# Optimization experiments

Hardware: AMD Instinct MI355X
Metric: run time of the kernel (lower is better)

The kernel has to match this reference:

```python
import jax, jax.numpy as jnp
import numpy as np


def _relative_position_index(ws: int) -> np.ndarray:
    # Matches torch meshgrid (ij) construction in _init_relative_positions.
    coords = np.stack(np.meshgrid(np.arange(ws), np.arange(ws), indexing='ij'), axis=0).reshape(2, -1)  # [2, ws*ws]
    rel = coords[:, :, None] - coords[:, None, :]          # [2, N, N]
    rel = rel.transpose(1, 2, 0).copy()                    # [N, N, 2]
    rel[:, :, 0] += ws - 1
    rel[:, :, 1] += ws - 1
    rel[:, :, 0] *= 2 * ws - 1
    return rel.sum(-1)                                     # [N, N] int


def setup_inputs() -> dict:
    key = jax.random.key(0)
    ks = jax.random.split(key, 6)
    B, N, C, H, WS = 4096, 49, 512, 16, 7
    x = jax.random.normal(ks[0], (B, N, C), dtype=jnp.float32)
    w_qkv = jax.random.normal(ks[1], (C, 3 * C), dtype=jnp.float32) * (C ** -0.5)
    b_qkv = jax.random.normal(ks[2], (3 * C,), dtype=jnp.float32) * 0.02
    w_proj = jax.random.normal(ks[3], (C, C), dtype=jnp.float32) * (C ** -0.5)
    b_proj = jax.random.normal(ks[4], (C,), dtype=jnp.float32) * 0.02
    bias_table = jax.random.normal(ks[5], ((2 * WS - 1) ** 2, H), dtype=jnp.float32) * 0.02
    return {"x": x, "w_qkv": w_qkv, "b_qkv": b_qkv, "w_proj": w_proj,
            "b_proj": b_proj, "bias_table": bias_table,
            "num_heads": H, "window_size": WS}


def reference(x, w_qkv, b_qkv, w_proj, b_proj, bias_table, num_heads, window_size):
    B, N, C = x.shape
    hd = C // num_heads
    qkv = (x @ w_qkv + b_qkv).reshape(B, N, 3, num_heads, hd)
    q, k, v = (qkv[:, :, i].transpose(0, 2, 1, 3) for i in range(3))  # each [B, H, N, hd]
    # NOTE: scale uses full channel dim C (as in source), not head_dim.
    attn = jnp.einsum('bhnd,bhmd->bhnm', q, k) * (C ** -0.5)          # [B, H, N, N]
    idx = _relative_position_index(window_size)                        # [N, N] static
    rel_bias = bias_table[idx].transpose(2, 0, 1)                      # [H, N, N]
    attn = jax.nn.softmax(attn + rel_bias[None], axis=-1)
    out = jnp.einsum('bhnm,bhmd->bhnd', attn, v)                       # [B, H, N, hd]
    out = out.transpose(0, 2, 1, 3).reshape(B, N, C)
    return out @ w_proj + b_proj
```

## Files before the change

kernel.cpp:

```cpp
#include <hip/hip_runtime.h>
#include <hip/hip_bf16.h>

typedef __attribute__((ext_vector_type(8))) short bf16x8;
typedef __attribute__((ext_vector_type(4))) float f32x4;

#define DEVI __device__ __forceinline__

DEVI short f2bf(float f) {
  union { float f; unsigned u; } v; v.f = f;
  unsigned r = v.u + 0x7FFFu + ((v.u >> 16) & 1u);
  return (short)(r >> 16);
}

DEVI void gl16(const void* g, void* l) {
  __builtin_amdgcn_global_load_lds((const __attribute__((address_space(1))) unsigned*)g,
                                   (__attribute__((address_space(3))) unsigned*)l,
                                   16, 0, 0);
}

DEVI float exp2a(float x) { float r; asm("v_exp_f32 %0, %1" : "=v"(r) : "v"(x)); return r; }

DEVI unsigned pk2(float lo, float hi) {
  union { __hip_bfloat162 h; unsigned u; } v;
  float2 f; f.x = lo; f.y = hi;
  v.h = __float22bfloat162_rn(f);
  return v.u;
}

union U8 { unsigned u[4]; bf16x8 v; };
DEVI bf16x8 mk8(unsigned a, unsigned b, unsigned c, unsigned d) {
  U8 x; x.u[0]=a; x.u[1]=b; x.u[2]=c; x.u[3]=d; return x.v;
}


__global__ __launch_bounds__(256) void conv_x_k(const float* __restrict__ x,
                                                short* __restrict__ xb) {
  long i = (long)blockIdx.x * 256 + threadIdx.x;
  const float4* xf = (const float4*)x;
  float4 a = xf[i * 2], c = xf[i * 2 + 1];
  bf16x8 r;
  r[0] = f2bf(a.x); r[1] = f2bf(a.y); r[2] = f2bf(a.z); r[3] = f2bf(a.w);
  r[4] = f2bf(c.x); r[5] = f2bf(c.y); r[6] = f2bf(c.z); r[7] = f2bf(c.w);
  *(bf16x8*)(xb + i * 8) = r;
}

__global__ __launch_bounds__(256) void conv_wT_k(const float* __restrict__ w,
                                                 short* __restrict__ wT, int Ncols) {
  int i = blockIdx.x * 256 + threadIdx.x;
  if (i >= Ncols * 512) return;
  int n = i >> 9, k = i & 511;
  wT[i] = f2bf(w[k * Ncols + n]);
}

__global__ __launch_bounds__(256) void fill_biasT(const float* __restrict__ btab,
                                                  float* __restrict__ biasT) {
  int i = blockIdx.x * 256 + threadIdx.x;
  int h = i >> 12, m = (i >> 6) & 63, n = i & 63;
  float v;
  if (m >= 49) {
    v = -1e30f;
  } else {
    int nn = n > 48 ? 48 : n;
    int ni = nn / 7, nj = nn - ni * 7;
    int mi = m / 7,  mj = m - mi * 7;
    int idx = (ni - mi + 6) * 13 + (nj - mj + 6);
    v = btab[idx * 16 + h] * 1.4426950408889634f;
  }
  biasT[i] = v;
}


template <int EPI>
__global__ __launch_bounds__(256, 2)
void gemm128(const short* __restrict__ A, const short* __restrict__ Bt,
             const float* __restrict__ bias, void* __restrict__ outp, int ctiles) {
  __shared__ short As[4096];
  __shared__ short Bs[4096];

  const int nwg = gridDim.x;
  const int w = blockIdx.x;
  const int chunk = nwg >> 3;
  const int tid = (w & 7) * chunk + (w >> 3);
  const int rt = tid / ctiles, ct = tid % ctiles;
  const long m0 = (long)rt * 128;
  const int n0 = ct * 128;

  const int t = threadIdx.x;
  const int lane = t & 63;
  const int wv = t >> 6;
  const int wm = wv >> 1, wn = wv & 1;
  const int l15 = lane & 15, g = lane >> 4;

  const int rA0 = t >> 2, cA = t & 3;
  const short* Ag0 = A + (m0 + rA0) * 512 + cA * 8;
  const short* Ag1 = A + (m0 + rA0 + 64) * 512 + cA * 8;
  const short* Bg0 = Bt + (long)(n0 + rA0) * 512 + cA * 8;
  const short* Bg1 = Bt + (long)(n0 + rA0 + 64) * 512 + cA * 8;
  short* Al0 = As + t * 8;
  short* Al1 = As + (t + 256) * 8;
  short* Bl0 = Bs + t * 8;
  short* Bl1 = Bs + (t + 256) * 8;

  const short* aRd = As + (wm * 64 + l15) * 32 + g * 8;
  const short* bRd = Bs + (wn * 64 + l15) * 32 + g * 8;

  f32x4 acc[4][4] = {};

  for (int kk = 0; kk < 512; kk += 32) {
    __syncthreads();
    gl16(Ag0 + kk, Al0);
    gl16(Ag1 + kk, Al1);
    gl16(Bg0 + kk, Bl0);
    gl16(Bg1 + kk, Bl1);
    __syncthreads();
    bf16x8 a[4], b[4];
#pragma unroll
    for (int i = 0; i < 4; ++i) a[i] = *(const bf16x8*)(aRd + i * 512);
#pragma unroll
    for (int j = 0; j < 4; ++j) b[j] = *(const bf16x8*)(bRd + j * 512);
#pragma unroll
    for (int i = 0; i < 4; ++i)
#pragma unroll
      for (int j = 0; j < 4; ++j)
        acc[i][j] = __builtin_amdgcn_mfma_f32_16x16x32_bf16(a[i], b[j], acc[i][j], 0, 0, 0);
  }

  if (EPI == 0) {
    short* qkv = (short*)outp;
#pragma unroll
    for (int i = 0; i < 4; ++i)
#pragma unroll
      for (int r = 0; r < 4; ++r) {
        int row = (int)m0 + wm * 64 + i * 16 + g * 4 + r;
        int b = row / 49, n = row - b * 49;
#pragma unroll
        for (int j = 0; j < 4; ++j) {
          int col = n0 + wn * 64 + j * 16 + l15;
          float val = acc[i][j][r] + bias[col];
          int ii = col >> 9, h = (col >> 5) & 15, d = col & 31;
          qkv[(long)((b * 16 + h) * 3 + ii) * 1568 + n * 32 + d] = f2bf(val);
        }
      }
  } else {
    float* out = (float*)outp;
#pragma unroll
    for (int i = 0; i < 4; ++i)
#pragma unroll
      for (int r = 0; r < 4; ++r) {
        long row = m0 + wm * 64 + i * 16 + g * 4 + r;
#pragma unroll
        for (int j = 0; j < 4; ++j) {
          int col = n0 + wn * 64 + j * 16 + l15;
          out[row * 512 + col] = acc[i][j][r] + bias[col];
        }
      }
  }
}


__global__ __launch_bounds__(256, 3)
void attn49(const short* __restrict__ qkvb, const float* __restrict__ biasT,
            short* __restrict__ ao) {
  const int t = threadIdx.x, lane = t & 63, wv = t >> 6;
  const int l15 = lane & 15, g = lane >> 4, g4 = g * 4;
  const int b = blockIdx.x >> 2;
  const int h = (blockIdx.x & 3) * 4 + wv;

  const short* qb = qkvb + (long)(b * 16 + h) * 3 * 1568;
  const short* kb = qb + 1568;
  const short* vb = kb + 1568;

  bf16x8 qf[4], kf[4];
#pragma unroll
  for (int i = 0; i < 4; ++i) {
    int row = i * 16 + l15; row = row > 48 ? 48 : row;
    kf[i] = *(const bf16x8*)(kb + row * 32 + g * 8);
    qf[i] = *(const bf16x8*)(qb + row * 32 + g * 8);
  }

  bf16x8 vf[2][2];
#pragma unroll
  for (int kt = 0; kt < 2; ++kt)
#pragma unroll
    for (int hi = 0; hi < 2; ++hi)
#pragma unroll
      for (int r = 0; r < 4; ++r) {
        int m = kt * 32 + hi * 16 + g4 + r;
        m = m > 48 ? 48 : m;
#pragma unroll
        for (int dt = 0; dt < 2; ++dt)
          vf[kt][dt][hi * 4 + r] = vb[m * 32 + dt * 16 + l15];
      }

  f32x4 s[4][4] = {};
#pragma unroll
  for (int i = 0; i < 4; ++i)
#pragma unroll
    for (int j = 0; j < 4; ++j)
      s[i][j] = __builtin_amdgcn_mfma_f32_16x16x32_bf16(kf[i], qf[j], s[i][j], 0, 0, 0);

  const float* biasH = biasT + h * 4096;
  float sum[4] = {0.f, 0.f, 0.f, 0.f};
#pragma unroll
  for (int i = 0; i < 4; ++i)
#pragma unroll
    for (int r = 0; r < 4; ++r) {
      int m = i * 16 + g4 + r;
      const float* bp = biasH + m * 64 + l15;
#pragma unroll
      for (int j = 0; j < 4; ++j) {
        float p = exp2a(fmaf(s[i][j][r], 0.06375871f, bp[j * 16]));
        s[i][j][r] = p;
        sum[j] += p;
      }
    }
#pragma unroll
  for (int j = 0; j < 4; ++j) {
    sum[j] += __shfl_xor(sum[j], 16);
    sum[j] += __shfl_xor(sum[j], 32);
    sum[j] = 1.f / sum[j];
  }

  unsigned pk[4][4][2];
#pragma unroll
  for (int j = 0; j < 4; ++j)
#pragma unroll
    for (int i = 0; i < 4; ++i) {
      pk[j][i][0] = pk2(s[i][j][0] * sum[j], s[i][j][1] * sum[j]);
      pk[j][i][1] = pk2(s[i][j][2] * sum[j], s[i][j][3] * sum[j]);
    }

  f32x4 o[4][2] = {};
#pragma unroll
  for (int j = 0; j < 4; ++j) {
    bf16x8 a0 = mk8(pk[j][0][0], pk[j][0][1], pk[j][1][0], pk[j][1][1]);
    bf16x8 a1 = mk8(pk[j][2][0], pk[j][2][1], pk[j][3][0], pk[j][3][1]);
    o[j][0] = __builtin_amdgcn_mfma_f32_16x16x32_bf16(a0, vf[0][0], o[j][0], 0, 0, 0);
    o[j][0] = __builtin_amdgcn_mfma_f32_16x16x32_bf16(a1, vf[1][0], o[j][0], 0, 0, 0);
    o[j][1] = __builtin_amdgcn_mfma_f32_16x16x32_bf16(a0, vf[0][1], o[j][1], 0, 0, 0);
    o[j][1] = __builtin_amdgcn_mfma_f32_16x16x32_bf16(a1, vf[1][1], o[j][1], 0, 0, 0);
  }

#pragma unroll
  for (int j = 0; j < 4; ++j)
#pragma unroll
    for (int r = 0; r < 4; ++r) {
      int n = j * 16 + g4 + r;
      if (n < 49) {
        long off = ((long)b * 49 + n) * 512 + h * 32 + l15;
        ao[off]      = f2bf(o[j][0][r]);
        ao[off + 16] = f2bf(o[j][1][r]);
      }
    }
}


extern "C" void kernel_launch(void* const* d_in, const int* in_sizes, int n_in,
                              void* d_out, int out_size, void* d_ws, size_t ws_size,
                              hipStream_t stream) {
  (void)in_sizes; (void)n_in; (void)out_size; (void)ws_size;
  const float* x      = (const float*)d_in[0];
  const float* w_qkv  = (const float*)d_in[1];
  const float* b_qkv  = (const float*)d_in[2];
  const float* w_proj = (const float*)d_in[3];
  const float* b_proj = (const float*)d_in[4];
  const float* btab   = (const float*)d_in[5];

  char* ws = (char*)d_ws;
  short* xb  = (short*)ws;
  short* wqT = (short*)(ws + 205520896L);
  short* wpT = (short*)(ws + 205520896L + 1572864L);
  short* qkv = (short*)(ws + 205520896L + 1572864L + 524288L);
  short* ao  = xb;
  float* biasT = (float*)wpT + 262144;
  biasT = (float*)wqT;

  conv_x_k <<<50176, 256, 0, stream>>>(x, xb);
  conv_wT_k<<<3072, 256, 0, stream>>>(w_qkv, wqT, 1536);
  conv_wT_k<<<1024, 256, 0, stream>>>(w_proj, wpT, 512);
  gemm128<0><<<18816, 256, 0, stream>>>(xb, wqT, b_qkv, (void*)qkv, 12);
  fill_biasT<<<256, 256, 0, stream>>>(btab, biasT);
  attn49   <<<16384, 256, 0, stream>>>(qkv, biasT, ao);
  gemm128<1><<<6272, 256, 0, stream>>>(ao, wpT, b_proj, d_out, 4);
}
```

Before: 949.3 us.

## Fuse QKV projection, window attention and output projection into one per-window kernel

Replaces the separate x conversion, QKV GEMM, attention and projection GEMM kernels with a single kernel that handles one window per block. x is converted to bf16 into swizzled LDS, each wave computes QKV for four heads and runs attention from LDS, then the attention output is written back to LDS for the projection GEMM. Weights are prepacked into MFMA fragment order and streamed directly from global/L2 per wave. This removes the HBM round trips for the bf16 x, qkv and attention output buffers. In exchange it pads 49 rows to 64, runs at low occupancy due to large LDS use, and generates heavy L2 weight traffic.

```diff
diff --git a/kernel.cpp b/kernel.cpp
--- a/kernel.cpp
+++ b/kernel.cpp
@@ -10,12 +10,6 @@
   union { float f; unsigned u; } v; v.f = f;
   unsigned r = v.u + 0x7FFFu + ((v.u >> 16) & 1u);
   return (short)(r >> 16);
-}
-
-DEVI void gl16(const void* g, void* l) {
-  __builtin_amdgcn_global_load_lds((const __attribute__((address_space(1))) unsigned*)g,
-                                   (__attribute__((address_space(3))) unsigned*)l,
-                                   16, 0, 0);
 }
 
 DEVI float exp2a(float x) { float r; asm("v_exp_f32 %0, %1" : "=v"(r) : "v"(x)); return r; }
@@ -32,24 +26,24 @@
   U8 x; x.u[0]=a; x.u[1]=b; x.u[2]=c; x.u[3]=d; return x.v;
 }
 
-
-__global__ __launch_bounds__(256) void conv_x_k(const float* __restrict__ x,
-                                                short* __restrict__ xb) {
-  long i = (long)blockIdx.x * 256 + threadIdx.x;
-  const float4* xf = (const float4*)x;
-  float4 a = xf[i * 2], c = xf[i * 2 + 1];
-  bf16x8 r;
-  r[0] = f2bf(a.x); r[1] = f2bf(a.y); r[2] = f2bf(a.z); r[3] = f2bf(a.w);
-  r[4] = f2bf(c.x); r[5] = f2bf(c.y); r[6] = f2bf(c.z); r[7] = f2bf(c.w);
-  *(bf16x8*)(xb + i * 8) = r;
-}
-
-__global__ __launch_bounds__(256) void conv_wT_k(const float* __restrict__ w,
-                                                 short* __restrict__ wT, int Ncols) {
+__global__ __launch_bounds__(256) void pack_wqkv(const float* __restrict__ w,
+                                                 short* __restrict__ wPk) {
   int i = blockIdx.x * 256 + threadIdx.x;
-  if (i >= Ncols * 512) return;
-  int n = i >> 9, k = i & 511;
-  wT[i] = f2bf(w[k * Ncols + n]);
+  int e = i & 7, lane = (i >> 3) & 63, kf = (i >> 9) & 15, hn = i >> 13;
+  int h = hn / 6, nf = hn - h * 6;
+  int g = lane >> 4, l15 = lane & 15;
+  int k = kf * 32 + g * 8 + e;
+  int col = (nf >> 1) * 512 + h * 32 + (nf & 1) * 16 + l15;
+  wPk[i] = f2bf(w[k * 1536 + col]);
+}
+
+__global__ __launch_bounds__(256) void pack_wproj(const float* __restrict__ w,
+                                                  short* __restrict__ wpPk) {
+  int i = blockIdx.x * 256 + threadIdx.x;
+  int e = i & 7, lane = (i >> 3) & 63, kf = (i >> 9) & 15, cf = i >> 13;
+  int g = lane >> 4, l15 = lane & 15;
+  int k = kf * 32 + g * 8 + e, col = cf * 16 + l15;
+  wpPk[i] = f2bf(w[k * 512 + col]);
 }
 
 __global__ __launch_bounds__(256) void fill_biasT(const float* __restrict__ btab,
@@ -70,186 +64,208 @@
 }
 
 
-template <int EPI>
-__global__ __launch_bounds__(256, 2)
-void gemm128(const short* __restrict__ A, const short* __restrict__ Bt,
-             const float* __restrict__ bias, void* __restrict__ outp, int ctiles) {
-  __shared__ short As[4096];
-  __shared__ short Bs[4096];
-
-  const int nwg = gridDim.x;
-  const int w = blockIdx.x;
-  const int chunk = nwg >> 3;
-  const int tid = (w & 7) * chunk + (w >> 3);
-  const int rt = tid / ctiles, ct = tid % ctiles;
-  const long m0 = (long)rt * 128;
-  const int n0 = ct * 128;
-
-  const int t = threadIdx.x;
-  const int lane = t & 63;
-  const int wv = t >> 6;
-  const int wm = wv >> 1, wn = wv & 1;
-  const int l15 = lane & 15, g = lane >> 4;
-
-  const int rA0 = t >> 2, cA = t & 3;
-  const short* Ag0 = A + (m0 + rA0) * 512 + cA * 8;
-  const short* Ag1 = A + (m0 + rA0 + 64) * 512 + cA * 8;
-  const short* Bg0 = Bt + (long)(n0 + rA0) * 512 + cA * 8;
-  const short* Bg1 = Bt + (long)(n0 + rA0 + 64) * 512 + cA * 8;
-  short* Al0 = As + t * 8;
-  short* Al1 = As + (t + 256) * 8;
-  short* Bl0 = Bs + t * 8;
-  short* Bl1 = Bs + (t + 256) * 8;
-
-  const short* aRd = As + (wm * 64 + l15) * 32 + g * 8;
-  const short* bRd = Bs + (wn * 64 + l15) * 32 + g * 8;
-
-  f32x4 acc[4][4] = {};
-
-  for (int kk = 0; kk < 512; kk += 32) {
-    __syncthreads();
-    gl16(Ag0 + kk, Al0);
-    gl16(Ag1 + kk, Al1);
-    gl16(Bg0 + kk, Bl0);
-    gl16(Bg1 + kk, Bl1);
-    __syncthreads();
-    bf16x8 a[4], b[4];
-#pragma unroll
-    for (int i = 0; i < 4; ++i) a[i] = *(const bf16x8*)(aRd + i * 512);
-#pragma unroll
-    for (int j = 0; j < 4; ++j) b[j] = *(const bf16x8*)(bRd + j * 512);
-#pragma unroll
-    for (int i = 0; i < 4; ++i)
-#pragma unroll
-      for (int j = 0; j < 4; ++j)
-        acc[i][j] = __builtin_amdgcn_mfma_f32_16x16x32_bf16(a[i], b[j], acc[i][j], 0, 0, 0);
-  }
-
-  if (EPI == 0) {
-    short* qkv = (short*)outp;
-#pragma unroll
-    for (int i = 0; i < 4; ++i)
-#pragma unroll
-      for (int r = 0; r < 4; ++r) {
-        int row = (int)m0 + wm * 64 + i * 16 + g * 4 + r;
-        int b = row / 49, n = row - b * 49;
-#pragma unroll
-        for (int j = 0; j < 4; ++j) {
-          int col = n0 + wn * 64 + j * 16 + l15;
-          float val = acc[i][j][r] + bias[col];
-          int ii = col >> 9, h = (col >> 5) & 15, d = col & 31;
-          qkv[(long)((b * 16 + h) * 3 + ii) * 1568 + n * 32 + d] = f2bf(val);
-        }
-      }
-  } else {
-    float* out = (float*)outp;
-#pragma unroll
-    for (int i = 0; i < 4; ++i)
-#pragma unroll
-      for (int r = 0; r < 4; ++r) {
-        long row = m0 + wm * 64 + i * 16 + g * 4 + r;
-#pragma unroll
-        for (int j = 0; j < 4; ++j) {
-          int col = n0 + wn * 64 + j * 16 + l15;
-          out[row * 512 + col] = acc[i][j][r] + bias[col];
-        }
-      }
-  }
-}
-
-
-__global__ __launch_bounds__(256, 3)
-void attn49(const short* __restrict__ qkvb, const float* __restrict__ biasT,
-            short* __restrict__ ao) {
+__global__ __launch_bounds__(256, 1)
+void fusedwin(const float* __restrict__ x, const short* __restrict__ wPk,
+              const short* __restrict__ wpPk, const float* __restrict__ bqkv,
+              const float* __restrict__ bproj, const float* __restrict__ biasT,
+              float* __restrict__ out) {
+  __shared__ short As[32768];
+  __shared__ short Bufs[4][6144];
+
   const int t = threadIdx.x, lane = t & 63, wv = t >> 6;
   const int l15 = lane & 15, g = lane >> 4, g4 = g * 4;
-  const int b = blockIdx.x >> 2;
-  const int h = (blockIdx.x & 3) * 4 + wv;
-
-  const short* qb = qkvb + (long)(b * 16 + h) * 3 * 1568;
-  const short* kb = qb + 1568;
-  const short* vb = kb + 1568;
-
-  bf16x8 qf[4], kf[4];
-#pragma unroll
-  for (int i = 0; i < 4; ++i) {
-    int row = i * 16 + l15; row = row > 48 ? 48 : row;
-    kf[i] = *(const bf16x8*)(kb + row * 32 + g * 8);
-    qf[i] = *(const bf16x8*)(qb + row * 32 + g * 8);
-  }
-
-  bf16x8 vf[2][2];
-#pragma unroll
-  for (int kt = 0; kt < 2; ++kt)
-#pragma unroll
-    for (int hi = 0; hi < 2; ++hi)
+  const int b = blockIdx.x;
+
+  {
+    const float* xw = x + (long)b * 25088;
+#pragma unroll
+    for (int it = 0; it < 16; ++it) {
+      int q = it * 256 + t, row = q >> 6, c = q & 63;
+      int sr = row > 48 ? 48 : row;
+      const float4* p = (const float4*)(xw + sr * 512 + c * 8);
+      float4 a = p[0], d = p[1];
+      bf16x8 r;
+      r[0] = f2bf(a.x); r[1] = f2bf(a.y); r[2] = f2bf(a.z); r[3] = f2bf(a.w);
+      r[4] = f2bf(d.x); r[5] = f2bf(d.y); r[6] = f2bf(d.z); r[7] = f2bf(d.w);
+      *(bf16x8*)(As + row * 512 + ((c ^ (row & 7)) * 8)) = r;
+    }
+  }
+  __syncthreads();
+
+  short* Qb = Bufs[wv];
+  short* Kb = Qb + 2048;
+  short* Vb = Qb + 4096;
+  const int x7 = l15 & 7;
+
+  unsigned up[4][4][2][2];
+
+#pragma unroll
+  for (int hh = 0; hh < 4; ++hh) {
+    const int h = wv * 4 + hh;
+
+    f32x4 acc[4][6] = {};
+    const short* wp = wPk + (long)(h * 96) * 512 + lane * 8;
+#pragma unroll
+    for (int kf = 0; kf < 16; ++kf) {
+      bf16x8 af[4], wf[6];
+#pragma unroll
+      for (int mf = 0; mf < 4; ++mf)
+        af[mf] = *(const bf16x8*)(As + (mf * 16 + l15) * 512 + (((kf * 4 + g) ^ x7) * 8));
+#pragma unroll
+      for (int nf = 0; nf < 6; ++nf)
+        wf[nf] = *(const bf16x8*)(wp + (nf * 16 + kf) * 512);
+#pragma unroll
+      for (int mf = 0; mf < 4; ++mf)
+#pragma unroll
+        for (int nf = 0; nf < 6; ++nf)
+          acc[mf][nf] = __builtin_amdgcn_mfma_f32_16x16x32_bf16(af[mf], wf[nf], acc[mf][nf], 0, 0, 0);
+    }
+
+#pragma unroll
+    for (int nf = 0; nf < 6; ++nf) {
+      float bq = bqkv[(nf >> 1) * 512 + h * 32 + (nf & 1) * 16 + l15];
+      short* buf = Qb + (nf >> 1) * 2048;
+      int d = (nf & 1) * 16 + l15;
+      int ch = d >> 3, d7 = d & 7;
+#pragma unroll
+      for (int mf = 0; mf < 4; ++mf)
+#pragma unroll
+        for (int r = 0; r < 4; ++r) {
+          int row = mf * 16 + g4 + r;
+          buf[row * 32 + ((ch ^ (row & 3)) * 8) + d7] = f2bf(acc[mf][nf][r] + bq);
+        }
+    }
+
+    bf16x8 qf[4], kfr[4];
+#pragma unroll
+    for (int i2 = 0; i2 < 4; ++i2) {
+      int row = i2 * 16 + l15;
+      int sl = (g ^ (row & 3)) * 8;
+      kfr[i2] = *(const bf16x8*)(Kb + row * 32 + sl);
+      qf[i2]  = *(const bf16x8*)(Qb + row * 32 + sl);
+    }
+    bf16x8 vf[2][2];
+#pragma unroll
+    for (int kt2 = 0; kt2 < 2; ++kt2)
+#pragma unroll
+      for (int hi = 0; hi < 2; ++hi)
+#pragma unroll
+        for (int r = 0; r < 4; ++r) {
+          int m = kt2 * 32 + hi * 16 + g4 + r;
+#pragma unroll
+          for (int dt = 0; dt < 2; ++dt) {
+            int d = dt * 16 + l15;
+            vf[kt2][dt][hi * 4 + r] = Vb[m * 32 + (((d >> 3) ^ (m & 3)) * 8) + (d & 7)];
+          }
+        }
+
+    f32x4 s[4][4] = {};
+#pragma unroll
+    for (int i2 = 0; i2 < 4; ++i2)
+#pragma unroll
+      for (int j = 0; j < 4; ++j)
+        s[i2][j] = __builtin_amdgcn_mfma_f32_16x16x32_bf16(kfr[i2], qf[j], s[i2][j], 0, 0, 0);
+
+    const float* biasH = biasT + h * 4096;
+    float sum[4] = {0.f, 0.f, 0.f, 0.f};
+#pragma unroll
+    for (int i2 = 0; i2 < 4; ++i2)
 #pragma unroll
       for (int r = 0; r < 4; ++r) {
-        int m = kt * 32 + hi * 16 + g4 + r;
-        m = m > 48 ? 48 : m;
-#pragma unroll
-        for (int dt = 0; dt < 2; ++dt)
-          vf[kt][dt][hi * 4 + r] = vb[m * 32 + dt * 16 + l15];
-      }
-
-  f32x4 s[4][4] = {};
-#pragma unroll
-  for (int i = 0; i < 4; ++i)
+        int m = i2 * 16 + g4 + r;
+        const float* bp = biasH + m * 64 + l15;
+#pragma unroll
+        for (int j = 0; j < 4; ++j) {
+          float p = exp2a(fmaf(s[i2][j][r], 0.06375871f, bp[j * 16]));
+          s[i2][j][r] = p;
+          sum[j] += p;
+        }
+      }
+#pragma unroll
+    for (int j = 0; j < 4; ++j) {
+      sum[j] += __shfl_xor(sum[j], 16);
+      sum[j] += __shfl_xor(sum[j], 32);
+      sum[j] = 1.f / sum[j];
+    }
+
+    unsigned pk[4][4][2];
 #pragma unroll
     for (int j = 0; j < 4; ++j)
-      s[i][j] = __builtin_amdgcn_mfma_f32_16x16x32_bf16(kf[i], qf[j], s[i][j], 0, 0, 0);
-
-  const float* biasH = biasT + h * 4096;
-  float sum[4] = {0.f, 0.f, 0.f, 0.f};
-#pragma unroll
-  for (int i = 0; i < 4; ++i)
+#pragma unroll
+      for (int i2 = 0; i2 < 4; ++i2) {
+        pk[j][i2][0] = pk2(s[i2][j][0] * sum[j], s[i2][j][1] * sum[j]);
+        pk[j][i2][1] = pk2(s[i2][j][2] * sum[j], s[i2][j][3] * sum[j]);
+      }
+
+    f32x4 o[4][2] = {};
+#pragma unroll
+    for (int j = 0; j < 4; ++j) {
+      bf16x8 a0 = mk8(pk[j][0][0], pk[j][0][1], pk[j][1][0], pk[j][1][1]);
+      bf16x8 a1 = mk8(pk[j][2][0], pk[j][2][1], pk[j][3][0], pk[j][3][1]);
+      o[j][0] = __builtin_amdgcn_mfma_f32_16x16x32_bf16(a0, vf[0][0], o[j][0], 0, 0, 0);
+      o[j][0] = __builtin_amdgcn_mfma_f32_16x16x32_bf16(a1, vf[1][0], o[j][0], 0, 0, 0);
+      o[j][1] = __builtin_amdgcn_mfma_f32_16x16x32_bf16(a0, vf[0][1], o[j][1], 0, 0, 0);
+      o[j][1] = __builtin_amdgcn_mfma_f32_16x16x32_bf16(a1, vf[1][1], o[j][1], 0, 0, 0);
+    }
+#pragma unroll
+    for (int j = 0; j < 4; ++j)
+#pragma unroll
+      for (int dt = 0; dt < 2; ++dt) {
+        up[hh][j][dt][0] = pk2(o[j][dt][0], o[j][dt][1]);
+        up[hh][j][dt][1] = pk2(o[j][dt][2], o[j][dt][3]);
+      }
+  }
+
+  __syncthreads();
+
+#pragma unroll
+  for (int hh = 0; hh < 4; ++hh) {
+    int h = wv * 4 + hh;
+#pragma unroll
+    for (int j = 0; j < 4; ++j)
+#pragma unroll
+      for (int r = 0; r < 4; ++r) {
+        int row = j * 16 + g4 + r;
+#pragma unroll
+        for (int dt = 0; dt < 2; ++dt) {
+          int col = h * 32 + dt * 16 + l15;
+          short val = (short)(up[hh][j][dt][r >> 1] >> ((r & 1) * 16));
+          As[row * 512 + (((col >> 3) ^ (row & 7)) * 8) + (col & 7)] = val;
+        }
+      }
+  }
+  __syncthreads();
+
+  f32x4 a2[4][8] = {};
+  const short* wpp = wpPk + (long)(wv * 128) * 512 + lane * 8;
+#pragma unroll
+  for (int kf = 0; kf < 16; ++kf) {
+    bf16x8 af2[4], wf2[8];
+#pragma unroll
+    for (int mf = 0; mf < 4; ++mf)
+      af2[mf] = *(const bf16x8*)(As + (mf * 16 + l15) * 512 + (((kf * 4 + g) ^ x7) * 8));
+#pragma unroll
+    for (int nf = 0; nf < 8; ++nf)
+      wf2[nf] = *(const bf16x8*)(wpp + (nf * 16 + kf) * 512);
+#pragma unroll
+    for (int mf = 0; mf < 4; ++mf)
+#pragma unroll
+      for (int nf = 0; nf < 8; ++nf)
+        a2[mf][nf] = __builtin_amdgcn_mfma_f32_16x16x32_bf16(af2[mf], wf2[nf], a2[mf][nf], 0, 0, 0);
+  }
+
+  float* ob = out + (long)b * 25088;
+#pragma unroll
+  for (int mf = 0; mf < 4; ++mf)
 #pragma unroll
     for (int r = 0; r < 4; ++r) {
-      int m = i * 16 + g4 + r;
-      const float* bp = biasH + m * 64 + l15;
-#pragma unroll
-      for (int j = 0; j < 4; ++j) {
-        float p = exp2a(fmaf(s[i][j][r], 0.06375871f, bp[j * 16]));
-        s[i][j][r] = p;
-        sum[j] += p;
-      }
-    }
-#pragma unroll
-  for (int j = 0; j < 4; ++j) {
-    sum[j] += __shfl_xor(sum[j], 16);
-    sum[j] += __shfl_xor(sum[j], 32);
-    sum[j] = 1.f / sum[j];
-  }
-
-  unsigned pk[4][4][2];
-#pragma unroll
-  for (int j = 0; j < 4; ++j)
-#pragma unroll
-    for (int i = 0; i < 4; ++i) {
-      pk[j][i][0] = pk2(s[i][j][0] * sum[j], s[i][j][1] * sum[j]);
-      pk[j][i][1] = pk2(s[i][j][2] * sum[j], s[i][j][3] * sum[j]);
-    }
-
-  f32x4 o[4][2] = {};
-#pragma unroll
-  for (int j = 0; j < 4; ++j) {
-    bf16x8 a0 = mk8(pk[j][0][0], pk[j][0][1], pk[j][1][0], pk[j][1][1]);
-    bf16x8 a1 = mk8(pk[j][2][0], pk[j][2][1], pk[j][3][0], pk[j][3][1]);
-    o[j][0] = __builtin_amdgcn_mfma_f32_16x16x32_bf16(a0, vf[0][0], o[j][0], 0, 0, 0);
-    o[j][0] = __builtin_amdgcn_mfma_f32_16x16x32_bf16(a1, vf[1][0], o[j][0], 0, 0, 0);
-    o[j][1] = __builtin_amdgcn_mfma_f32_16x16x32_bf16(a0, vf[0][1], o[j][1], 0, 0, 0);
-    o[j][1] = __builtin_amdgcn_mfma_f32_16x16x32_bf16(a1, vf[1][1], o[j][1], 0, 0, 0);
-  }
-
-#pragma unroll
-  for (int j = 0; j < 4; ++j)
-#pragma unroll
-    for (int r = 0; r < 4; ++r) {
-      int n = j * 16 + g4 + r;
-      if (n < 49) {
-        long off = ((long)b * 49 + n) * 512 + h * 32 + l15;
-        ao[off]      = f2bf(o[j][0][r]);
-        ao[off + 16] = f2bf(o[j][1][r]);
+      int row = mf * 16 + g4 + r;
+      if (row < 49) {
+#pragma unroll
+        for (int nf = 0; nf < 8; ++nf) {
+          int col = wv * 128 + nf * 16 + l15;
+          ob[row * 512 + col] = a2[mf][nf][r] + bproj[col];
+        }
       }
     }
 }
@@ -267,19 +283,13 @@
   const float* btab   = (const float*)d_in[5];
 
   char* ws = (char*)d_ws;
-  short* xb  = (short*)ws;
-  short* wqT = (short*)(ws + 205520896L);
-  short* wpT = (short*)(ws + 205520896L + 1572864L);
-  short* qkv = (short*)(ws + 205520896L + 1572864L + 524288L);
-  short* ao  = xb;
-  float* biasT = (float*)wpT + 262144;
-  biasT = (float*)wqT;
-
-  conv_x_k <<<50176, 256, 0, stream>>>(x, xb);
-  conv_wT_k<<<3072, 256, 0, stream>>>(w_qkv, wqT, 1536);
-  conv_wT_k<<<1024, 256, 0, stream>>>(w_proj, wpT, 512);
-  gemm128<0><<<18816, 256, 0, stream>>>(xb, wqT, b_qkv, (void*)qkv, 12);
+  short* wPk   = (short*)ws;
+  short* wpPk  = (short*)(ws + 1572864L);
+  float* biasT = (float*)(ws + 1572864L + 524288L);
+
+  pack_wqkv <<<3072, 256, 0, stream>>>(w_qkv, wPk);
+  pack_wproj<<<1024, 256, 0, stream>>>(w_proj, wpPk);
   fill_biasT<<<256, 256, 0, stream>>>(btab, biasT);
-  attn49   <<<16384, 256, 0, stream>>>(qkv, biasT, ao);
-  gemm128<1><<<6272, 256, 0, stream>>>(ao, wpT, b_proj, d_out, 4);
-}
+  fusedwin  <<<4096, 256, 0, stream>>>(x, wPk, wpPk, b_qkv, b_proj, biasT,
+                                       (float*)d_out);
+}
```

Measured after the change: 1.510 ms. 1.59x slower.
